# Kernel optimization log

Hardware: AMD Instinct MI355X
Metric: run time of the kernel (lower is better)

The kernel has to match this reference:

```python
import jax, jax.numpy as jnp
import numpy as np

EPS = 1e-5

def layer_norm(x, g, b):
    mu = jnp.mean(x, axis=-1, keepdims=True)
    var = jnp.var(x, axis=-1, keepdims=True)
    return (x - mu) * jax.lax.rsqrt(var + EPS) * g + b

def setup_inputs() -> dict:
    key = jax.random.key(0)
    ks = jax.random.split(key, 16)
    N, E, D, ED = 50000, 500000, 128, 5
    def w(k, i, o):
        return jax.random.normal(k, (i, o), jnp.float32) / np.sqrt(i)
    return {
        "x": jax.random.normal(ks[0], (N, D), jnp.float32),
        "edge_attr": jax.random.normal(ks[1], (E, ED), jnp.float32),
        "pos": jax.random.normal(ks[2], (N, 3), jnp.float32),
        "node_w1": w(ks[3], D, D), "node_b1": jnp.zeros((D,), jnp.float32),
        "node_g1": jnp.ones((D,), jnp.float32), "node_be1": jnp.zeros((D,), jnp.float32),
        "node_w2": w(ks[4], D, D), "node_b2": jnp.zeros((D,), jnp.float32),
        "edge_w1": w(ks[5], 2 * D + ED, D), "edge_b1": jnp.zeros((D,), jnp.float32),
        "edge_g1": jnp.ones((D,), jnp.float32), "edge_be1": jnp.zeros((D,), jnp.float32),
        "edge_w2": w(ks[6], D, D), "edge_b2": jnp.zeros((D,), jnp.float32),
        "upd_w": w(ks[7], 2 * D, D), "upd_b": jnp.zeros((D,), jnp.float32),
        "ln_g": jnp.ones((D,), jnp.float32), "ln_b": jnp.zeros((D,), jnp.float32),
        "edge_index": jax.random.randint(ks[8], (2, E), 0, N, jnp.int64),
    }

def reference(x, edge_attr, pos, node_w1, node_b1, node_g1, node_be1, node_w2, node_b2,
              edge_w1, edge_b1, edge_g1, edge_be1, edge_w2, edge_b2,
              upd_w, upd_b, ln_g, ln_b, edge_index):
    N = x.shape[0]
    # node MLP: Linear -> LayerNorm -> ReLU -> Linear (dropout=0)
    h_nodes = jax.nn.relu(layer_norm(x @ node_w1 + node_b1, node_g1, node_be1)) @ node_w2 + node_b2
    src, dst = edge_index[0], edge_index[1]
    # edge MLP on gathered endpoint features + edge_attr  [E, 2D+edge_dim]
    ef = jnp.concatenate([x[src], x[dst], edge_attr], axis=1)
    h_edges = jax.nn.relu(layer_norm(ef @ edge_w1 + edge_b1, edge_g1, edge_be1)) @ edge_w2 + edge_b2
    # scatter-add aggregation to destination nodes
    h_agg = jax.ops.segment_sum(h_edges, dst, num_segments=N)
    h_out = jnp.concatenate([h_nodes, h_agg], axis=1) @ upd_w + upd_b
    h_out = h_out + x  # residual (in_channels == out_channels)
    return layer_norm(h_out, ln_g, ln_b)
```

## Files before the change

### kernel.cpp

```cpp
#include <hip/hip_runtime.h>
#include <stdint.h>

#define D    128
#define ED   5
#define BLK  512
#define WPB  8
#define W1S  296
#define W2S  136
#define HS   136
#define US   264
#define GRID 256

typedef __attribute__((ext_vector_type(8))) short bf16x8;
typedef __attribute__((ext_vector_type(4))) float f32x4;

__device__ __forceinline__ unsigned short f2bf(float f) {
    union { float f; uint32_t u; } c; c.f = f;
    uint32_t r = (c.u + 0x7fffu + ((c.u >> 16) & 1u)) >> 16;
    return (unsigned short)r;
}
__device__ __forceinline__ float bflo(uint32_t u) {
    union { uint32_t u; float f; } c; c.u = u << 16; return c.f;
}
__device__ __forceinline__ float bfhi(uint32_t u) {
    union { uint32_t u; float f; } c; c.u = u & 0xffff0000u; return c.f;
}
__device__ __forceinline__ bf16x8 cvt8(const float* __restrict__ p) {
    float4 a = *(const float4*)p;
    float4 b = *(const float4*)(p + 4);
    bf16x8 r;
    r[0] = (short)f2bf(a.x); r[1] = (short)f2bf(a.y);
    r[2] = (short)f2bf(a.z); r[3] = (short)f2bf(a.w);
    r[4] = (short)f2bf(b.x); r[5] = (short)f2bf(b.y);
    r[6] = (short)f2bf(b.z); r[7] = (short)f2bf(b.w);
    return r;
}
__device__ __forceinline__ bool detect64(const int* ei) {
    return (ei[1] == 0) & (ei[3] == 0) & (ei[5] == 0) &
           (ei[7] == 0) & (ei[9] == 0) & (ei[11] == 0);
}

__global__ __launch_bounds__(256)
void cvt_x_kernel(const float* __restrict__ in, unsigned short* __restrict__ out, int n8) {
    int i = blockIdx.x * blockDim.x + threadIdx.x;
    if (i >= n8) return;
    float4 a = ((const float4*)in)[2 * i];
    float4 b = ((const float4*)in)[2 * i + 1];
    union { unsigned short s[8]; uint4 v; } p;
    p.s[0] = f2bf(a.x); p.s[1] = f2bf(a.y); p.s[2] = f2bf(a.z); p.s[3] = f2bf(a.w);
    p.s[4] = f2bf(b.x); p.s[5] = f2bf(b.y); p.s[6] = f2bf(b.z); p.s[7] = f2bf(b.w);
    ((uint4*)out)[i] = p.v;
}

__global__ __launch_bounds__(512)
void count_kernel(const int* __restrict__ ei, int* __restrict__ cnt, int E) {
    const bool is64 = detect64(ei);
    int e = blockIdx.x * 512 + threadIdx.x;
    if (e >= E) return;
    int d = is64 ? ei[2 * ((size_t)E + e)] : ei[(size_t)E + e];
    atomicAdd(&cnt[d], 1);
}

__global__ __launch_bounds__(1024)
void scan_blk_kernel(const int* __restrict__ cnt, int* __restrict__ part,
                     int* __restrict__ bsum, int N) {
    __shared__ int wsum[16];
    const int tid = threadIdx.x, wave = tid >> 6, lane = tid & 63;
    const int idx = blockIdx.x * 1024 + tid;
    int v = (idx < N) ? cnt[idx] : 0;
    int s = v;
    #pragma unroll
    for (int off = 1; off < 64; off <<= 1) {
        int t = __shfl_up(s, off, 64);
        if (lane >= off) s += t;
    }
    if (lane == 63) wsum[wave] = s;
    __syncthreads();
    if (wave == 0 && lane < 16) {
        int ws_ = wsum[lane];
        #pragma unroll
        for (int off = 1; off < 16; off <<= 1) {
            int t = __shfl_up(ws_, off, 64);
            if (lane >= off) ws_ += t;
        }
        wsum[lane] = ws_;
    }
    __syncthreads();
    const int excl = ((wave == 0) ? 0 : wsum[wave - 1]) + (s - v);
    if (idx < N) part[idx] = excl;
    if (tid == 0) bsum[blockIdx.x] = wsum[15];
}

__global__ __launch_bounds__(1024)
void scan_top_kernel(int* __restrict__ bsum, int nb) {
    __shared__ int wsum[16];
    const int tid = threadIdx.x, wave = tid >> 6, lane = tid & 63;
    int v = (tid < nb) ? bsum[tid] : 0;
    int s = v;
    #pragma unroll
    for (int off = 1; off < 64; off <<= 1) {
        int t = __shfl_up(s, off, 64);
        if (lane >= off) s += t;
    }
    if (lane == 63) wsum[wave] = s;
    __syncthreads();
    if (wave == 0 && lane < 16) {
        int ws_ = wsum[lane];
        #pragma unroll
        for (int off = 1; off < 16; off <<= 1) {
            int t = __shfl_up(ws_, off, 64);
            if (lane >= off) ws_ += t;
        }
        wsum[lane] = ws_;
    }
    __syncthreads();
    const int excl = ((wave == 0) ? 0 : wsum[wave - 1]) + (s - v);
    if (tid < nb) bsum[tid] = excl;
}

__global__ __launch_bounds__(1024)
void scan_add_kernel(const int* __restrict__ part, const int* __restrict__ bsum,
                     int* __restrict__ starts, int* __restrict__ cursor,
                     int N, int E) {
    const int idx = blockIdx.x * 1024 + threadIdx.x;
    if (idx < N) {
        int v = part[idx] + bsum[blockIdx.x];
        starts[idx] = v;
        cursor[idx] = v;
    }
    if (blockIdx.x == 0 && threadIdx.x == 0) starts[N] = E;
}

__global__ __launch_bounds__(512)
void fill_kernel(const int* __restrict__ ei, int* __restrict__ cursor,
                 int* __restrict__ slotp, int E) {
    const bool is64 = detect64(ei);
    int e = blockIdx.x * 512 + threadIdx.x;
    if (e >= E) return;
    int d = is64 ? ei[2 * ((size_t)E + e)] : ei[(size_t)E + e];
    slotp[e] = atomicAdd(&cursor[d], 1);
}

__global__ __launch_bounds__(512)
void agg_kernel(const unsigned short* __restrict__ h2, const int* __restrict__ starts,
                unsigned short* __restrict__ aggb, int N) {
    const int wid = blockIdx.x * WPB + (threadIdx.x >> 6);
    if (wid >= N) return;
    const int lane = threadIdx.x & 63;
    const int s = starts[wid], t = starts[wid + 1];
    const unsigned short* p = h2 + (size_t)s * D + 2 * lane;
    const int n = t - s;
    float a0 = 0.f, a1 = 0.f, b0 = 0.f, b1 = 0.f;
    float p0 = 0.f, p1 = 0.f, q0 = 0.f, q1 = 0.f;
    int j = 0;
    for (; j + 4 <= n; j += 4) {
        uint32_t u0 = *(const uint32_t*)(p + (size_t)(j + 0) * D);
        uint32_t u1 = *(const uint32_t*)(p + (size_t)(j + 1) * D);
        uint32_t u2 = *(const uint32_t*)(p + (size_t)(j + 2) * D);
        uint32_t u3 = *(const uint32_t*)(p + (size_t)(j + 3) * D);
        a0 += bflo(u0); a1 += bfhi(u0);
        b0 += bflo(u1); b1 += bfhi(u1);
        p0 += bflo(u2); p1 += bfhi(u2);
        q0 += bflo(u3); q1 += bfhi(u3);
    }
    for (; j < n; ++j) {
        uint32_t u = *(const uint32_t*)(p + (size_t)j * D);
        a0 += bflo(u); a1 += bfhi(u);
    }
    const float r0 = (a0 + b0) + (p0 + q0);
    const float r1 = (a1 + b1) + (p1 + q1);
    uint32_t o = (uint32_t)f2bf(r0) | ((uint32_t)f2bf(r1) << 16);
    *(uint32_t*)(aggb + (size_t)wid * D + 2 * lane) = o;
}

template<bool EDGE, bool XBF, bool CSR>
__global__ __launch_bounds__(BLK, 2)
void mlp_kernel(const float* __restrict__ x, const unsigned short* __restrict__ xbf,
                const float* __restrict__ ea, const int* __restrict__ ei,
                const int* __restrict__ slotp,
                const float* __restrict__ w1, const float* __restrict__ b1,
                const float* __restrict__ g1, const float* __restrict__ be1,
                const float* __restrict__ w2, const float* __restrict__ b2,
                unsigned short* __restrict__ hout, float* __restrict__ aggf,
                int N, int E)
{
    __shared__ unsigned short w1t[128 * W1S];
    __shared__ unsigned short w2t[128 * W2S];
    __shared__ unsigned short hb[WPB][16 * HS];

    const int tid = threadIdx.x;
    const int KROWS = EDGE ? 288 : 128;
    for (int i = tid; i < KROWS * 128; i += BLK) {
        int k = i >> 7, n = i & 127;
        float v = (!EDGE || k < (2 * D + ED)) ? w1[k * 128 + n] : 0.f;
        w1t[n * W1S + k] = f2bf(v);
    }
    for (int i = tid; i < 128 * 128; i += BLK) {
        int k = i >> 7, n = i & 127;
        w2t[n * W2S + k] = f2bf(w2[k * 128 + n]);
    }
    __syncthreads();

    bool is64 = false;
    if (EDGE) is64 = detect64(ei);

    const int lane = tid & 63, w = tid >> 6;
    const int g = lane >> 4, c = lane & 15;

    float b1v[8], g1v[8], e1v[8], b2v[8];
    #pragma unroll
    for (int nt = 0; nt < 8; ++nt) {
        b1v[nt] = b1[nt * 16 + c];  g1v[nt] = g1[nt * 16 + c];
        e1v[nt] = be1[nt * 16 + c]; b2v[nt] = b2[nt * 16 + c];
    }

    const int cnt = EDGE ? E : N;
    const int nT = (cnt + 15) >> 4;
    const int step = gridDim.x * WPB;
    unsigned short* hw = hb[w];

    int pdd = 0, prc = 0, psl = 0;
    size_t paoff = 0, pboff = 0;
    bf16x8 pf[9];

    auto loadIdx = [&](int tl) {
        const int rr = tl * 16 + c;
        const int rc = rr < cnt ? rr : cnt - 1;
        prc = rc;
        if (EDGE) {
            int s = is64 ? ei[2 * (size_t)rc]       : ei[rc];
            pdd   = is64 ? ei[2 * ((size_t)E + rc)] : ei[(size_t)E + rc];
            paoff = (size_t)s * D;
            pboff = (size_t)pdd * D;
            if (CSR) psl = slotp[rc];
        } else {
            paoff = (size_t)rc * D;
        }
    };
    auto loadFrags = [&]() {
        #pragma unroll
        for (int kk = 0; kk < (EDGE ? 8 : 4); ++kk) {
            const size_t o = (kk < 4) ? paoff + kk * 32 : pboff + (kk - 4) * 32;
            if (XBF) pf[kk] = *(const bf16x8*)(xbf + o + 8 * g);
            else     pf[kk] = cvt8(x + o + 8 * g);
        }
        if (EDGE) {
            bf16x8 t;
            #pragma unroll
            for (int j = 0; j < 8; ++j) t[j] = 0;
            if (g == 0) {
                #pragma unroll
                for (int j = 0; j < ED; ++j)
                    t[j] = (short)f2bf(ea[(size_t)prc * ED + j]);
            }
            pf[8] = t;
        }
    };

    int tile = blockIdx.x * WPB + w;
    if (tile < nT) { loadIdx(tile); loadFrags(); }

    for (; tile < nT; tile += step) {
        bf16x8 af[9];
        #pragma unroll
        for (int kk = 0; kk < (EDGE ? 9 : 4); ++kk) af[kk] = pf[kk];
        const int dd = pdd;
        const int sl = psl;
        const int row = tile * 16 + c;

        const int tn = tile + step;
        loadIdx(tn < nT ? tn : tile);

        const f32x4 z = {0.f, 0.f, 0.f, 0.f};
        f32x4 acc[8] = {z, z, z, z, z, z, z, z};
        #pragma unroll
        for (int kk = 0; kk < (EDGE ? 9 : 4); ++kk) {
            const unsigned short* wr = &w1t[c * W1S + kk * 32 + 8 * g];
            #pragma unroll
            for (int nt = 0; nt < 8; ++nt) {
                bf16x8 bf = *(const bf16x8*)(wr + nt * 16 * W1S);
                acc[nt] = __builtin_amdgcn_mfma_f32_16x16x32_bf16(af[kk], bf, acc[nt], 0, 0, 0);
            }
        }

        loadFrags();

        float mean[4], rstd[4];
        #pragma unroll
        for (int r = 0; r < 4; ++r) {
            float s = 0.f, q = 0.f;
            #pragma unroll
            for (int nt = 0; nt < 8; ++nt) {
                float v = acc[nt][r] + b1v[nt];
                acc[nt][r] = v;
                s += v; q += v * v;
            }
            s += __shfl_xor(s, 1, 64); q += __shfl_xor(q, 1, 64);
            s += __shfl_xor(s, 2, 64); q += __shfl_xor(q, 2, 64);
            s += __shfl_xor(s, 4, 64); q += __shfl_xor(q, 4, 64);
            s += __shfl_xor(s, 8, 64); q += __shfl_xor(q, 8, 64);
            float m = s * (1.f / 128.f);
            float var = q * (1.f / 128.f) - m * m;
            mean[r] = m;
            rstd[r] = rsqrtf(var + 1e-5f);
        }
        #pragma unroll
        for (int nt = 0; nt < 8; ++nt) {
            #pragma unroll
            for (int r = 0; r < 4; ++r) {
                float h = fmaxf((acc[nt][r] - mean[r]) * rstd[r] * g1v[nt] + e1v[nt], 0.f);
                const int rw = 4 * g + r;
                hw[rw * HS + ((nt * 2 + (c >> 3)) ^ ((rw >> 1) & 7)) * 8 + (c & 7)] = f2bf(h);
            }
        }

        f32x4 acc2[8] = {z, z, z, z, z, z, z, z};
        #pragma unroll
        for (int kk = 0; kk < 4; ++kk) {
            bf16x8 hf = *(const bf16x8*)&hw[c * HS + ((4 * kk + g) ^ ((c >> 1) & 7)) * 8];
            const unsigned short* wr = &w2t[c * W2S + kk * 32 + 8 * g];
            #pragma unroll
            for (int nt = 0; nt < 8; ++nt) {
                bf16x8 bf = *(const bf16x8*)(wr + nt * 16 * W2S);
                acc2[nt] = __builtin_amdgcn_mfma_f32_16x16x32_bf16(hf, bf, acc2[nt], 0, 0, 0);
            }
        }

        if (EDGE && !CSR) {
            int dv[4];
            #pragma unroll
            for (int r = 0; r < 4; ++r) dv[r] = __shfl(dd, 4 * g + r, 64);
            #pragma unroll
            for (int r = 0; r < 4; ++r) {
                const int er = tile * 16 + 4 * g + r;
                if (er < cnt) {
                    float* dst = aggf + (size_t)dv[r] * D + c;
                    #pragma unroll
                    for (int nt = 0; nt < 8; ++nt)
                        atomicAdd(dst + nt * 16, acc2[nt][r] + b2v[nt]);
                }
            }
        } else {
            #pragma unroll
            for (int nt = 0; nt < 8; ++nt) {
                #pragma unroll
                for (int r = 0; r < 4; ++r) {
                    const int rw = 4 * g + r;
                    hw[rw * HS + ((nt * 2 + (c >> 3)) ^ ((rw >> 1) & 7)) * 8 + (c & 7)] =
                        f2bf(acc2[nt][r] + b2v[nt]);
                }
            }
            if (row < cnt) {
                const int orow = (EDGE && CSR) ? sl : row;
                unsigned short* dst = hout + (size_t)orow * D;
                #pragma unroll
                for (int j = 0; j < 4; ++j)
                    *(uint4*)(dst + (j * 4 + g) * 8) =
                        *(const uint4*)&hw[c * HS + ((j * 4 + g) ^ ((c >> 1) & 7)) * 8];
            }
        }
    }
}

template<bool AGGBF, bool XBF>
__global__ __launch_bounds__(BLK, 4)
void upd2_kernel(const unsigned short* __restrict__ hnb, const void* __restrict__ aggp,
                 const float* __restrict__ x, const unsigned short* __restrict__ xbf,
                 const float* __restrict__ uw, const float* __restrict__ ub,
                 const float* __restrict__ lg, const float* __restrict__ lb,
                 float* __restrict__ out, int N)
{
    __shared__ unsigned short wt[128 * US];
    const int tid = threadIdx.x;
    for (int i = tid; i < 256 * 128; i += BLK) {
        int k = i >> 7, n = i & 127;
        wt[n * US + k] = f2bf(uw[i]);
    }
    __syncthreads();

    const int lane = tid & 63, w = tid >> 6;
    const int g = lane >> 4, c = lane & 15;

    float ubv[8], gv[8], bv[8];
    #pragma unroll
    for (int nt = 0; nt < 8; ++nt) {
        ubv[nt] = ub[nt * 16 + c]; gv[nt] = lg[nt * 16 + c]; bv[nt] = lb[nt * 16 + c];
    }

    const int nT = (N + 15) >> 4;
    for (int tile = blockIdx.x * WPB + w; tile < nT; tile += gridDim.x * WPB) {
        const int row = tile * 16 + c;
        const int rc  = row < N ? row : N - 1;

        const f32x4 z = {0.f, 0.f, 0.f, 0.f};
        f32x4 acc[8] = {z, z, z, z, z, z, z, z};

        #pragma unroll
        for (int kk = 0; kk < 8; ++kk) {
            bf16x8 af;
            if (kk < 4) {
                af = *(const bf16x8*)(hnb + (size_t)rc * D + kk * 32 + 8 * g);
            } else {
                if (AGGBF)
                    af = *(const bf16x8*)((const unsigned short*)aggp +
                                          (size_t)rc * D + (kk - 4) * 32 + 8 * g);
                else
                    af = cvt8((const float*)aggp + (size_t)rc * D + (kk - 4) * 32 + 8 * g);
            }
            const unsigned short* wr = &wt[c * US + kk * 32 + 8 * g];
            #pragma unroll
            for (int nt = 0; nt < 8; ++nt) {
                bf16x8 bf = *(const bf16x8*)(wr + nt * 16 * US);
                acc[nt] = __builtin_amdgcn_mfma_f32_16x16x32_bf16(af, bf, acc[nt], 0, 0, 0);
            }
        }

        float mean[4], rstd[4];
        #pragma unroll
        for (int r = 0; r < 4; ++r) {
            const int row4 = tile * 16 + 4 * g + r;
            const int r4c = row4 < N ? row4 : N - 1;
            float s = 0.f, q = 0.f;
            #pragma unroll
            for (int nt = 0; nt < 8; ++nt) {
                float xr;
                if (XBF) xr = bflo((uint32_t)xbf[(size_t)r4c * D + nt * 16 + c]);
                else     xr = x[(size_t)r4c * D + nt * 16 + c];
                float v = acc[nt][r] + ubv[nt] + xr;
                acc[nt][r] = v;
                s += v; q += v * v;
            }
            s += __shfl_xor(s, 1, 64); q += __shfl_xor(q, 1, 64);
            s += __shfl_xor(s, 2, 64); q += __shfl_xor(q, 2, 64);
            s += __shfl_xor(s, 4, 64); q += __shfl_xor(q, 4, 64);
            s += __shfl_xor(s, 8, 64); q += __shfl_xor(q, 8, 64);
            float m = s * (1.f / 128.f);
            mean[r] = m;
            rstd[r] = rsqrtf(q * (1.f / 128.f) - m * m + 1e-5f);
        }
        #pragma unroll
        for (int r = 0; r < 4; ++r) {
            const int row4 = tile * 16 + 4 * g + r;
            if (row4 < N) {
                #pragma unroll
                for (int nt = 0; nt < 8; ++nt)
                    out[(size_t)row4 * D + nt * 16 + c] =
                        (acc[nt][r] - mean[r]) * rstd[r] * gv[nt] + bv[nt];
            }
        }
    }
}

extern "C" void kernel_launch(void* const* d_in, const int* in_sizes, int n_in,
                              void* d_out, int out_size, void* d_ws, size_t ws_size,
                              hipStream_t stream)
{
    const float* x    = (const float*)d_in[0];
    const float* ea   = (const float*)d_in[1];
    const float* nw1  = (const float*)d_in[3];
    const float* nb1  = (const float*)d_in[4];
    const float* ng1  = (const float*)d_in[5];
    const float* nbe1 = (const float*)d_in[6];
    const float* nw2  = (const float*)d_in[7];
    const float* nb2  = (const float*)d_in[8];
    const float* ew1  = (const float*)d_in[9];
    const float* eb1  = (const float*)d_in[10];
    const float* eg1  = (const float*)d_in[11];
    const float* ebe1 = (const float*)d_in[12];
    const float* ew2  = (const float*)d_in[13];
    const float* eb2  = (const float*)d_in[14];
    const float* uw   = (const float*)d_in[15];
    const float* ub   = (const float*)d_in[16];
    const float* lg   = (const float*)d_in[17];
    const float* lb   = (const float*)d_in[18];
    const int*   eidx = (const int*)d_in[19];

    const int N = in_sizes[0] / D;
    const int E = in_sizes[1] / ED;

    char* base = (char*)d_ws;
    size_t off = 0;
    auto alloc = [&](size_t bytes) -> char* {
        char* p = base + off;
        off = (off + bytes + 255) & ~(size_t)255;
        return p;
    };

    unsigned short* hnb  = (unsigned short*)alloc((size_t)N * D * 2);
    unsigned short* aggb = (unsigned short*)alloc((size_t)N * D * 2);
    unsigned short* xbf  = (unsigned short*)alloc((size_t)N * D * 2);
    int* cnt    = (int*)alloc((size_t)N * 4);
    int* starts = (int*)alloc(((size_t)N + 1) * 4);
    int* cursor = (int*)alloc((size_t)N * 4);
    int* bsum   = (int*)alloc(1024 * 4);
    int* slotA  = (int*)alloc((size_t)E * 4);
    unsigned short* h2 = (unsigned short*)alloc((size_t)E * D * 2);
    const size_t needA = off;

    const int n8 = N * D / 8;
    const int egrid = (E + 511) / 512;
    const int nb = (N + 1023) / 1024;
    const int ugrid = (((N + 15) / 16) + WPB - 1) / WPB;

    if (ws_size >= needA && nb <= 1024) {
        hipMemsetAsync(cnt, 0, (size_t)N * 4, stream);
        cvt_x_kernel<<<(n8 + 255) / 256, 256, 0, stream>>>(x, xbf, n8);
        count_kernel<<<egrid, 512, 0, stream>>>(eidx, cnt, E);
        scan_blk_kernel<<<nb, 1024, 0, stream>>>(cnt, cursor, bsum, N);
        scan_top_kernel<<<1, 1024, 0, stream>>>(bsum, nb);
        scan_add_kernel<<<nb, 1024, 0, stream>>>(cursor, bsum, starts, cursor, N, E);
        fill_kernel<<<egrid, 512, 0, stream>>>(eidx, cursor, slotA, E);
        mlp_kernel<false, true, true><<<GRID, BLK, 0, stream>>>(
            x, xbf, nullptr, nullptr, nullptr, nw1, nb1, ng1, nbe1, nw2, nb2,
            hnb, nullptr, N, E);
        mlp_kernel<true, true, true><<<GRID, BLK, 0, stream>>>(
            x, xbf, ea, eidx, slotA, ew1, eb1, eg1, ebe1, ew2, eb2,
            h2, nullptr, N, E);
        agg_kernel<<<(N + WPB - 1) / WPB, 512, 0, stream>>>(h2, starts, aggb, N);
        upd2_kernel<true, true><<<ugrid, BLK, 0, stream>>>(
            hnb, aggb, x, xbf, uw, ub, lg, lb, (float*)d_out, N);
        return;
    }

    off = 0;
    unsigned short* hnb2 = (unsigned short*)alloc((size_t)N * D * 2);
    float* aggf = (float*)alloc((size_t)N * D * 4);
    unsigned short* xbf2 = (unsigned short*)alloc((size_t)N * D * 2);
    const size_t needB = off;

    hipMemsetAsync(aggf, 0, (size_t)N * D * 4, stream);
    if (ws_size >= needB) {
        cvt_x_kernel<<<(n8 + 255) / 256, 256, 0, stream>>>(x, xbf2, n8);
        mlp_kernel<false, true, false><<<GRID, BLK, 0, stream>>>(
            x, xbf2, nullptr, nullptr, nullptr, nw1, nb1, ng1, nbe1, nw2, nb2,
            hnb2, nullptr, N, E);
        mlp_kernel<true, true, false><<<GRID, BLK, 0, stream>>>(
            x, xbf2, ea, eidx, nullptr, ew1, eb1, eg1, ebe1, ew2, eb2,
            nullptr, aggf, N, E);
        upd2_kernel<false, true><<<ugrid, BLK, 0, stream>>>(
            hnb2, aggf, x, xbf2, uw, ub, lg, lb, (float*)d_out, N);
    } else {
        mlp_kernel<false, false, false><<<GRID, BLK, 0, stream>>>(
            x, nullptr, nullptr, nullptr, nullptr, nw1, nb1, ng1, nbe1, nw2, nb2,
            hnb2, nullptr, N, E);
        mlp_kernel<true, false, false><<<GRID, BLK, 0, stream>>>(
            x, nullptr, ea, eidx, nullptr, ew1, eb1, eg1, ebe1, ew2, eb2,
            nullptr, aggf, N, E);
        upd2_kernel<false, false><<<ugrid, BLK, 0, stream>>>(
            hnb2, aggf, x, nullptr, uw, ub, lg, lb, (float*)d_out, N);
    }
}
```

Before: 469.6 us.

## Process edges in destination-sorted order and fuse cast with degree count

The fill kernel now writes a CSR edge-id permutation instead of per-edge output slots. The edge MLP walks edges in destination-sorted order: it gathers the source/destination indices and edge_attr through that permutation and writes h2 rows sequentially. The aim is better locality for the x[dst] gathers and coalesced output writes, at the price of an extra indirection and scattered reads of edge_index and edge_attr. The x bf16 conversion and the degree count are fused into one launch, and the XOR swizzle on the LDS hidden buffer is dropped, which may bring back bank conflicts.

Measured after the change: 472.1 us. No clear change (+0.5%).

```diff
diff --git a/kernel.cpp b/kernel.cpp
--- a/kernel.cpp
+++ b/kernel.cpp
@@ -40,25 +40,25 @@
            (ei[7] == 0) & (ei[9] == 0) & (ei[11] == 0);
 }
 
-__global__ __launch_bounds__(256)
-void cvt_x_kernel(const float* __restrict__ in, unsigned short* __restrict__ out, int n8) {
-    int i = blockIdx.x * blockDim.x + threadIdx.x;
-    if (i >= n8) return;
-    float4 a = ((const float4*)in)[2 * i];
-    float4 b = ((const float4*)in)[2 * i + 1];
-    union { unsigned short s[8]; uint4 v; } p;
-    p.s[0] = f2bf(a.x); p.s[1] = f2bf(a.y); p.s[2] = f2bf(a.z); p.s[3] = f2bf(a.w);
-    p.s[4] = f2bf(b.x); p.s[5] = f2bf(b.y); p.s[6] = f2bf(b.z); p.s[7] = f2bf(b.w);
-    ((uint4*)out)[i] = p.v;
-}
-
 __global__ __launch_bounds__(512)
-void count_kernel(const int* __restrict__ ei, int* __restrict__ cnt, int E) {
-    const bool is64 = detect64(ei);
-    int e = blockIdx.x * 512 + threadIdx.x;
-    if (e >= E) return;
-    int d = is64 ? ei[2 * ((size_t)E + e)] : ei[(size_t)E + e];
-    atomicAdd(&cnt[d], 1);
+void cvt_count_kernel(const float* __restrict__ in, unsigned short* __restrict__ out,
+                      int n8, const int* __restrict__ ei, int* __restrict__ cnt, int E) {
+    const int i = blockIdx.x * 512 + threadIdx.x;
+    if (i < n8) {
+        float4 a = ((const float4*)in)[2 * i];
+        float4 b = ((const float4*)in)[2 * i + 1];
+        union { unsigned short s[8]; uint4 v; } p;
+        p.s[0] = f2bf(a.x); p.s[1] = f2bf(a.y); p.s[2] = f2bf(a.z); p.s[3] = f2bf(a.w);
+        p.s[4] = f2bf(b.x); p.s[5] = f2bf(b.y); p.s[6] = f2bf(b.z); p.s[7] = f2bf(b.w);
+        ((uint4*)out)[i] = p.v;
+    } else {
+        const int e = i - n8;
+        if (e < E) {
+            const bool is64 = detect64(ei);
+            int d = is64 ? ei[2 * ((size_t)E + e)] : ei[(size_t)E + e];
+            atomicAdd(&cnt[d], 1);
+        }
+    }
 }
 
 __global__ __launch_bounds__(1024)
@@ -133,12 +133,13 @@
 
 __global__ __launch_bounds__(512)
 void fill_kernel(const int* __restrict__ ei, int* __restrict__ cursor,
-                 int* __restrict__ slotp, int E) {
+                 int* __restrict__ eids, int E) {
     const bool is64 = detect64(ei);
     int e = blockIdx.x * 512 + threadIdx.x;
     if (e >= E) return;
     int d = is64 ? ei[2 * ((size_t)E + e)] : ei[(size_t)E + e];
-    slotp[e] = atomicAdd(&cursor[d], 1);
+    int pos = atomicAdd(&cursor[d], 1);
+    eids[pos] = e;
 }
 
 __global__ __launch_bounds__(512)
@@ -177,7 +178,7 @@
 __global__ __launch_bounds__(BLK, 2)
 void mlp_kernel(const float* __restrict__ x, const unsigned short* __restrict__ xbf,
                 const float* __restrict__ ea, const int* __restrict__ ei,
-                const int* __restrict__ slotp,
+                const int* __restrict__ eids,
                 const float* __restrict__ w1, const float* __restrict__ b1,
                 const float* __restrict__ g1, const float* __restrict__ be1,
                 const float* __restrict__ w2, const float* __restrict__ b2,
@@ -219,21 +220,22 @@
     const int step = gridDim.x * WPB;
     unsigned short* hw = hb[w];
 
-    int pdd = 0, prc = 0, psl = 0;
+    int pdd = 0, pe = 0;
     size_t paoff = 0, pboff = 0;
     bf16x8 pf[9];
 
     auto loadIdx = [&](int tl) {
         const int rr = tl * 16 + c;
         const int rc = rr < cnt ? rr : cnt - 1;
-        prc = rc;
         if (EDGE) {
-            int s = is64 ? ei[2 * (size_t)rc]       : ei[rc];
-            pdd   = is64 ? ei[2 * ((size_t)E + rc)] : ei[(size_t)E + rc];
+            const int e = CSR ? eids[rc] : rc;
+            pe = e;
+            int s = is64 ? ei[2 * (size_t)e]       : ei[e];
+            pdd   = is64 ? ei[2 * ((size_t)E + e)] : ei[(size_t)E + e];
             paoff = (size_t)s * D;
             pboff = (size_t)pdd * D;
-            if (CSR) psl = slotp[rc];
         } else {
+            pe = rc;
             paoff = (size_t)rc * D;
         }
     };
@@ -251,7 +253,7 @@
             if (g == 0) {
                 #pragma unroll
                 for (int j = 0; j < ED; ++j)
-                    t[j] = (short)f2bf(ea[(size_t)prc * ED + j]);
+                    t[j] = (short)f2bf(ea[(size_t)pe * ED + j]);
             }
             pf[8] = t;
         }
@@ -265,7 +267,6 @@
         #pragma unroll
         for (int kk = 0; kk < (EDGE ? 9 : 4); ++kk) af[kk] = pf[kk];
         const int dd = pdd;
-        const int sl = psl;
         const int row = tile * 16 + c;
 
         const int tn = tile + step;
@@ -309,15 +310,14 @@
             #pragma unroll
             for (int r = 0; r < 4; ++r) {
                 float h = fmaxf((acc[nt][r] - mean[r]) * rstd[r] * g1v[nt] + e1v[nt], 0.f);
-                const int rw = 4 * g + r;
-                hw[rw * HS + ((nt * 2 + (c >> 3)) ^ ((rw >> 1) & 7)) * 8 + (c & 7)] = f2bf(h);
+                hw[(4 * g + r) * HS + nt * 16 + c] = f2bf(h);
             }
         }
 
         f32x4 acc2[8] = {z, z, z, z, z, z, z, z};
         #pragma unroll
         for (int kk = 0; kk < 4; ++kk) {
-            bf16x8 hf = *(const bf16x8*)&hw[c * HS + ((4 * kk + g) ^ ((c >> 1) & 7)) * 8];
+            bf16x8 hf = *(const bf16x8*)&hw[c * HS + kk * 32 + 8 * g];
             const unsigned short* wr = &w2t[c * W2S + kk * 32 + 8 * g];
             #pragma unroll
             for (int nt = 0; nt < 8; ++nt) {
@@ -344,19 +344,15 @@
             #pragma unroll
             for (int nt = 0; nt < 8; ++nt) {
                 #pragma unroll
-                for (int r = 0; r < 4; ++r) {
-                    const int rw = 4 * g + r;
-                    hw[rw * HS + ((nt * 2 + (c >> 3)) ^ ((rw >> 1) & 7)) * 8 + (c & 7)] =
-                        f2bf(acc2[nt][r] + b2v[nt]);
-                }
+                for (int r = 0; r < 4; ++r)
+                    hw[(4 * g + r) * HS + nt * 16 + c] = f2bf(acc2[nt][r] + b2v[nt]);
             }
             if (row < cnt) {
-                const int orow = (EDGE && CSR) ? sl : row;
-                unsigned short* dst = hout + (size_t)orow * D;
+                unsigned short* dst = hout + (size_t)row * D;
                 #pragma unroll
                 for (int j = 0; j < 4; ++j)
                     *(uint4*)(dst + (j * 4 + g) * 8) =
-                        *(const uint4*)&hw[c * HS + ((j * 4 + g) ^ ((c >> 1) & 7)) * 8];
+                        *(const uint4*)&hw[c * HS + (j * 4 + g) * 8];
             }
         }
     }
@@ -493,7 +489,7 @@
     int* starts = (int*)alloc(((size_t)N + 1) * 4);
     int* cursor = (int*)alloc((size_t)N * 4);
     int* bsum   = (int*)alloc(1024 * 4);
-    int* slotA  = (int*)alloc((size_t)E * 4);
+    int* eids   = (int*)alloc((size_t)E * 4);
     unsigned short* h2 = (unsigned short*)alloc((size_t)E * D * 2);
     const size_t needA = off;
 
@@ -504,17 +500,17 @@
 
     if (ws_size >= needA && nb <= 1024) {
         hipMemsetAsync(cnt, 0, (size_t)N * 4, stream);
-        cvt_x_kernel<<<(n8 + 255) / 256, 256, 0, stream>>>(x, xbf, n8);
-        count_kernel<<<egrid, 512, 0, stream>>>(eidx, cnt, E);
+        cvt_count_kernel<<<(n8 + E + 511) / 512, 512, 0, stream>>>(
+            x, xbf, n8, eidx, cnt, E);
         scan_blk_kernel<<<nb, 1024, 0, stream>>>(cnt, cursor, bsum, N);
         scan_top_kernel<<<1, 1024, 0, stream>>>(bsum, nb);
         scan_add_kernel<<<nb, 1024, 0, stream>>>(cursor, bsum, starts, cursor, N, E);
-        fill_kernel<<<egrid, 512, 0, stream>>>(eidx, cursor, slotA, E);
+        fill_kernel<<<egrid, 512, 0, stream>>>(eidx, cursor, eids, E);
         mlp_kernel<false, true, true><<<GRID, BLK, 0, stream>>>(
             x, xbf, nullptr, nullptr, nullptr, nw1, nb1, ng1, nbe1, nw2, nb2,
             hnb, nullptr, N, E);
         mlp_kernel<true, true, true><<<GRID, BLK, 0, stream>>>(
-            x, xbf, ea, eidx, slotA, ew1, eb1, eg1, ebe1, ew2, eb2,
+            x, xbf, ea, eidx, eids, ew1, eb1, eg1, ebe1, ew2, eb2,
             h2, nullptr, N, E);
         agg_kernel<<<(N + WPB - 1) / WPB, 512, 0, stream>>>(h2, starts, aggb, N);
         upd2_kernel<true, true><<<ugrid, BLK, 0, stream>>>(
@@ -530,7 +526,8 @@
 
     hipMemsetAsync(aggf, 0, (size_t)N * D * 4, stream);
     if (ws_size >= needB) {
-        cvt_x_kernel<<<(n8 + 255) / 256, 256, 0, stream>>>(x, xbf2, n8);
+        cvt_count_kernel<<<(n8 + 511) / 512, 512, 0, stream>>>(
+            x, xbf2, n8, nullptr, nullptr, 0);
         mlp_kernel<false, true, false><<<GRID, BLK, 0, stream>>>(
             x, xbf2, nullptr, nullptr, nullptr, nw1, nb1, ng1, nbe1, nw2, nb2,
             hnb2, nullptr, N, E);
```
